# Performance work log

Hardware: AMD Instinct MI355X
Metric: run time of the kernel (lower is better)

The kernel has to match this reference:

```python
import jax, jax.numpy as jnp
import numpy as np

N = 16384
FPS_RATIO = 0.5
RADIUS = 0.25
MAX_NEIGHBORS = 10
C_IN, C_HID, C_OUT = 3, 64, 128


def setup_inputs() -> dict:
    key = jax.random.key(0)
    k0, k1, k2 = jax.random.split(key, 3)
    pos = jax.random.uniform(k0, (N, 3), dtype=jnp.float32)
    batch = jnp.zeros((N,), dtype=jnp.int32)  # single point cloud
    W1 = jax.random.normal(k1, (C_IN, C_HID), dtype=jnp.float32) / np.float32(np.sqrt(C_IN))
    b1 = jnp.zeros((C_HID,), jnp.float32)
    W2 = jax.random.normal(k2, (C_HID, C_OUT), dtype=jnp.float32) / np.float32(np.sqrt(C_HID))
    b2 = jnp.zeros((C_OUT,), jnp.float32)
    return {"pos": pos, "batch": batch, "W1": W1, "b1": b1, "W2": W2, "b2": b2}


def _fps(pos, n_samples):
    # iterative farthest point sampling, deterministic start at index 0
    n = pos.shape[0]
    init = (jnp.full((n,), jnp.finfo(jnp.float32).max, jnp.float32), jnp.int32(0))
    def step(carry, _):
        min_d, last = carry
        d = jnp.sum((pos - pos[last]) ** 2, axis=-1)
        min_d = jnp.minimum(min_d, d)
        nxt = jnp.argmax(min_d).astype(jnp.int32)
        return (min_d, nxt), last
    _, idx = jax.lax.scan(step, init, None, length=n_samples)
    return idx


def _forward(pos, W1, b1, W2, b2):
    n = pos.shape[0]
    s = int(n * FPS_RATIO)
    idx = jax.lax.stop_gradient(_fps(pos, s))          # [S] sampled centers
    centers = pos[idx]                                  # [S,3]
    # ball query: squared distances from each center to all points  [S,N]
    d2 = jnp.sum((centers[:, None, :] - pos[None, :, :]) ** 2, axis=-1)
    neg_d2, src = jax.lax.top_k(-d2, MAX_NEIGHBORS)     # [S,K] nearest-first
    valid = neg_d2 >= -(RADIUS ** 2)                    # within the ball
    # edge_index = stack([col, row]): source = src (full-set idx),
    # target = row (sampled-set idx in [0,S)). PointNetConv does pos_i = pos[row],
    # i.e. indexes the FULL pos with sampled-set indices -> pos[:s].
    pos_i = pos[:s]                                     # [S,3]
    rel = pos[src] - pos_i[:, None, :]                  # [S,K,3] pos_j - pos_i
    # local_mlp (Linear->ReLU->Linear) on each edge message
    h = jax.nn.relu(rel @ W1 + b1) @ W2 + b2            # [S,K,C_OUT]
    h = jnp.where(valid[..., None], h, jnp.float32(-jnp.inf))
    tgt = jnp.repeat(jnp.arange(s, dtype=jnp.int32), MAX_NEIGHBORS)
    out = jax.ops.segment_max(h.reshape(-1, C_OUT), tgt, num_segments=n)  # [N,C]
    # nodes with no incoming edges -> 0 (PyG scatter-max empty fill)
    return jnp.where(jnp.isfinite(out), out, jnp.float32(0.0))


def reference(pos, batch, W1, b1, W2, b2):
    return _forward(pos, W1, b1, W2, b2)
```

## Files before the change

kernel.cpp:

```cpp
#include <hip/hip_runtime.h>

typedef unsigned int u32;
typedef unsigned long long u64;
typedef float f32x2 __attribute__((ext_vector_type(2)));

#define N_PTS 16384
#define N_S   8192
#define NB    10
#define CHID  64
#define COUT  128
#define R2    0.0625f
#define NCELL 4096

__device__ __forceinline__ u32 spread3(u32 v) {
  return (v & 1u) | ((v & 2u) << 2) | ((v & 4u) << 4) | ((v & 8u) << 6);
}

__global__ void cell_kernel(const float* __restrict__ pos, int* __restrict__ cellid,
                            int* __restrict__ hist) {
  int i = blockIdx.x * 256 + threadIdx.x;
  float x = pos[3 * i], y = pos[3 * i + 1], z = pos[3 * i + 2];
  u32 ix = (u32)(x * 16.0f); if (ix > 15u) ix = 15u;
  u32 iy = (u32)(y * 16.0f); if (iy > 15u) iy = 15u;
  u32 iz = (u32)(z * 16.0f); if (iz > 15u) iz = 15u;
  u32 c = spread3(ix) | (spread3(iy) << 1) | (spread3(iz) << 2);
  cellid[i] = (int)c;
  atomicAdd(&hist[c], 1);
}

__global__ __launch_bounds__(1024) void scan_kernel(const int* __restrict__ hist,
                                                    int* __restrict__ base) {
  __shared__ int sp[1024];
  int t = threadIdx.x;
  int h0 = hist[4 * t], h1 = hist[4 * t + 1], h2 = hist[4 * t + 2], h3 = hist[4 * t + 3];
  int s = h0 + h1 + h2 + h3;
  int acc = s;
  sp[t] = s;
  __syncthreads();
  for (int off = 1; off < 1024; off <<= 1) {
    int v = (t >= off) ? sp[t - off] : 0;
    __syncthreads();
    acc += v;
    sp[t] = acc;
    __syncthreads();
  }
  int excl = acc - s;
  base[4 * t + 0] = excl;
  base[4 * t + 1] = excl + h0;
  base[4 * t + 2] = excl + h0 + h1;
  base[4 * t + 3] = excl + h0 + h1 + h2;
}

__global__ void scatter_kernel(const float* __restrict__ pos, const int* __restrict__ cellid,
                               int* __restrict__ base, float* __restrict__ xs,
                               float* __restrict__ ys, float* __restrict__ zs,
                               int* __restrict__ oid) {
  int i = blockIdx.x * 256 + threadIdx.x;
  int c = cellid[i];
  int d = atomicAdd(&base[c], 1);
  xs[d] = pos[3 * i]; ys[d] = pos[3 * i + 1]; zs[d] = pos[3 * i + 2];
  oid[d] = i;
}

#define FPS_T 1024
#define PPT   16
#define WRK   192
#define NCHK  (N_S / 32)

#define OFF_SK   131072
#define OFF_SPD  16384
#define OFF_SPI  57472
#define OFF_W2T  98560
#define OFF_W1   133376
#define OFF_B1   134144
#define OFF_PROG 134400
#define SMEM_SZ  134432

#define KNS    32
#define KTILE  1024
#define KPAD   321
#define W2S    68

#define PT_LIST(OP) OP(0) OP(1) OP(2) OP(3) OP(4) OP(5) OP(6) OP(7) \
                    OP(8) OP(9) OP(10) OP(11) OP(12) OP(13) OP(14) OP(15)
#define G4_LIST(OP) OP(0,0,1,2,3,0,1)   OP(1,4,5,6,7,2,3) \
                    OP(2,8,9,10,11,4,5) OP(3,12,13,14,15,6,7)
#define PR_LIST(OP) OP(0) OP(1) OP(2) OP(3) OP(4) OP(5) OP(6) OP(7)

__device__ __forceinline__ u64 u64fmax(u64 a, u64 b) {
  double ad = __longlong_as_double((long long)a);
  double bd = __longlong_as_double((long long)b);
  return (u64)(long long)__double_as_longlong(fmax(ad, bd));
}

template <int CTRL, int RM>
__device__ __forceinline__ u64 dppmax(u64 cur) {
  int slo = __builtin_amdgcn_update_dpp(0, (int)(u32)cur, CTRL, RM, 0xf, false);
  int shi = __builtin_amdgcn_update_dpp(0, (int)(u32)(cur >> 32), CTRL, RM, 0xf, false);
  u64 o = ((u64)(u32)shi << 32) | (u32)slo;
  return u64fmax(o, cur);
}

__device__ __forceinline__ f32x2 pk_add(f32x2 a, f32x2 b) {
  f32x2 d;
  asm("v_pk_add_f32 %0, %1, %2" : "=v"(d) : "v"(a), "v"(b));
  return d;
}
__device__ __forceinline__ f32x2 pk_mul(f32x2 a, f32x2 b) {
  f32x2 d;
  asm("v_pk_mul_f32 %0, %1, %2" : "=v"(d) : "v"(a), "v"(b));
  return d;
}

__global__ __launch_bounds__(1024, 4)
void fused_kernel(const float* __restrict__ pos,
                  const float* __restrict__ xs,
                  const float* __restrict__ ys,
                  const float* __restrict__ zs,
                  const int* __restrict__ oidv,
                  int* __restrict__ idx,
                  int* __restrict__ src,
                  int* __restrict__ valid,
                  const float* __restrict__ W1,
                  const float* __restrict__ b1,
                  const float* __restrict__ W2,
                  const float* __restrict__ b2,
                  float* __restrict__ out,
                  int* __restrict__ prog) {
  __shared__ __align__(16) unsigned char smem[SMEM_SZ];
  const int t = threadIdx.x;

  if (blockIdx.x == 0) {
    float2* s_yz = (float2*)smem;
    u64 (*s_k)[16] = (u64 (*)[16])(smem + OFF_SK);
    const int wv = t >> 6;
    const int base0 = t * PPT;
    const float4* __restrict__ xv = (const float4*)(xs + base0);
    const float4* __restrict__ yv = (const float4*)(ys + base0);
    const float4* __restrict__ zv = (const float4*)(zs + base0);
    const int4*   __restrict__ ov = (const int4*)(oidv + base0);

#define DECLP(J) float md##J;
    PT_LIST(DECLP)
#undef DECLP
#define DECLC(J) u32 C##J;
    PT_LIST(DECLC)
#undef DECLC
#define DECLX(P) f32x2 X##P; f32x2 Y##P; f32x2 Z##P;
    PR_LIST(DECLX)
#undef DECLX

    float bnx = 3.4e38f, bxx = -3.4e38f, bny = 3.4e38f, bxy = -3.4e38f,
          bnz = 3.4e38f, bxz = -3.4e38f;

#define INIT4(G, J0, J1, J2, J3, PA, PB) { \
    float4 vx = xv[G], vy = yv[G], vz = zv[G]; int4 vo = ov[G]; \
    md##J0 = 3.402823466e38f; md##J1 = 3.402823466e38f; \
    md##J2 = 3.402823466e38f; md##J3 = 3.402823466e38f; \
    X##PA.x = vx.x; X##PA.y = vx.y; X##PB.x = vx.z; X##PB.y = vx.w; \
    Y##PA.x = vy.x; Y##PA.y = vy.y; Y##PB.x = vy.z; Y##PB.y = vy.w; \
    Z##PA.x = vz.x; Z##PA.y = vz.y; Z##PB.x = vz.z; Z##PB.y = vz.w; \
    s_yz[J0 * FPS_T + t] = make_float2(vy.x, vz.x); \
    s_yz[J1 * FPS_T + t] = make_float2(vy.y, vz.y); \
    s_yz[J2 * FPS_T + t] = make_float2(vy.z, vz.z); \
    s_yz[J3 * FPS_T + t] = make_float2(vy.w, vz.w); \
    C##J0 = ((16383u - (u32)vo.x) << 14) | (u32)(base0 + J0); \
    C##J1 = ((16383u - (u32)vo.y) << 14) | (u32)(base0 + J1); \
    C##J2 = ((16383u - (u32)vo.z) << 14) | (u32)(base0 + J2); \
    C##J3 = ((16383u - (u32)vo.w) << 14) | (u32)(base0 + J3); \
    bnx = fminf(bnx, fminf(fminf(vx.x, vx.y), fminf(vx.z, vx.w))); \
    bxx = fmaxf(bxx, fmaxf(fmaxf(vx.x, vx.y), fmaxf(vx.z, vx.w))); \
    bny = fminf(bny, fminf(fminf(vy.x, vy.y), fminf(vy.z, vy.w))); \
    bxy = fmaxf(bxy, fmaxf(fmaxf(vy.x, vy.y), fmaxf(vy.z, vy.w))); \
    bnz = fminf(bnz, fminf(fminf(vz.x, vz.y), fminf(vz.z, vz.w))); \
    bxz = fmaxf(bxz, fmaxf(fmaxf(vz.x, vz.y), fmaxf(vz.z, vz.w))); }
    G4_LIST(INIT4)
#undef INIT4

    u64 ckey = 0;
    u64 wklast = 0;
    float cmaxf = 3.402823466e38f;
    float cx = pos[0], cy = pos[1], cz = pos[2];
    if (t == 0) idx[0] = 0;
    __syncthreads();

    for (int k = 0; k < N_S - 1; ++k) {
      float dxl = fmaxf(fmaxf(bnx - cx, cx - bxx), 0.0f);
      float dyl = fmaxf(fmaxf(bny - cy, cy - bxy), 0.0f);
      float dzl = fmaxf(fmaxf(bnz - cz, cz - bxz), 0.0f);
      float lb2 = dxl * dxl + dyl * dyl + dzl * dzl;
      bool act = (0.99f * lb2 < cmaxf);

      if (__ballot(act)) {
        if (act) {
          f32x2 ncx2; ncx2.x = -cx; ncx2.y = -cx;
          f32x2 ncy2; ncy2.x = -cy; ncy2.y = -cy;
          f32x2 ncz2; ncz2.x = -cz; ncz2.y = -cz;
          u64 bkA = 0, bkB = 0;
#define UPDP(P, J0, J1) { \
          f32x2 dx2 = pk_add(X##P, ncx2); \
          f32x2 dy2 = pk_add(Y##P, ncy2); \
          f32x2 dz2 = pk_add(Z##P, ncz2); \
          f32x2 sq = pk_add(pk_mul(dx2, dx2), pk_mul(dy2, dy2)); \
          f32x2 d2 = pk_add(sq, pk_mul(dz2, dz2)); \
          float m0 = fminf(md##J0, d2.x); md##J0 = m0; \
          bkA = u64fmax(bkA, ((u64)__float_as_uint(m0) << 32) | C##J0); \
          float m1 = fminf(md##J1, d2.y); md##J1 = m1; \
          bkB = u64fmax(bkB, ((u64)__float_as_uint(m1) << 32) | C##J1); }
          UPDP(0, 0, 1)  UPDP(1, 2, 3)  UPDP(2, 4, 5)  UPDP(3, 6, 7)
          UPDP(4, 8, 9)  UPDP(5, 10, 11) UPDP(6, 12, 13) UPDP(7, 14, 15)
#undef UPDP
          ckey = u64fmax(bkA, bkB);
          cmaxf = __uint_as_float((u32)(ckey >> 32));
        }
        u64 wk = ckey;
        wk = dppmax<0x111, 0xf>(wk);
        wk = dppmax<0x112, 0xf>(wk);
        wk = dppmax<0x114, 0xf>(wk);
        wk = dppmax<0x118, 0xf>(wk);
        wk = dppmax<0x142, 0xa>(wk);
        wk = dppmax<0x143, 0xc>(wk);
        wklast = wk;
      }
      if ((t & 63) == 63) s_k[k & 1][wv] = wklast;
      __syncthreads();

      u64 gk = s_k[k & 1][t & 15];
      gk = dppmax<0x121, 0xf>(gk);
      gk = dppmax<0x122, 0xf>(gk);
      gk = dppmax<0x124, 0xf>(gk);
      gk = dppmax<0x128, 0xf>(gk);
      u32 glo = (u32)__builtin_amdgcn_readfirstlane((int)(u32)gk);
      u32 ghi = (u32)__builtin_amdgcn_readfirstlane((int)(u32)(gk >> 32));
      u64 gmax = ((u64)ghi << 32) | glo;
      int sidx = (int)(gmax & 16383u);
      if (t == 0) {
        idx[k + 1] = 16383 - (int)((gmax >> 14) & 16383u);
        if ((k & 31) == 30)
          __hip_atomic_store(prog, k + 2, __ATOMIC_RELEASE, __HIP_MEMORY_SCOPE_AGENT);
      }
      int cell = (sidx & (PPT - 1)) * FPS_T + (sidx >> 4);
      cx = xs[sidx];
      float2 yz = s_yz[cell];
      cy = yz.x;
      cz = yz.y;
    }
  } else {
    const int wid = blockIdx.x - 1;
    float4* s_p = (float4*)smem;
    float (*spd)[KPAD] = (float (*)[KPAD])(smem + OFF_SPD);
    int   (*spi)[KPAD] = (int (*)[KPAD])(smem + OFF_SPI);
    float* sW2T = (float*)(smem + OFF_W2T);
    float* sW1  = (float*)(smem + OFF_W1);
    float* sb1  = (float*)(smem + OFF_B1);
    int*   sprog = (int*)(smem + OFF_PROG);
    float* msh1  = (float*)(smem + OFF_SPD);
    float* msrel = (float*)(smem + OFF_SPI);

    for (int e = t; e < CHID * COUT; e += 1024) {
      int kk = e >> 7, c = e & (COUT - 1);
      sW2T[c * W2S + kk] = W2[e];
    }
    if (t < 3 * CHID) sW1[t] = W1[t];
    if (t < CHID) sb1[t] = b1[t];
    {
      float4* outv = (float4*)(out + (size_t)N_S * COUT);
      const int cnt = (N_PTS - N_S) * COUT / 4;
      for (int j = wid * 1024 + t; j < cnt; j += WRK * 1024)
        outv[j] = make_float4(0.f, 0.f, 0.f, 0.f);
    }
    __syncthreads();

    for (int gc = wid; gc < NCHK; gc += WRK) {
      const int need = gc * 32 + 32;
      for (;;) {
        if (t == 0) *sprog = __hip_atomic_load(prog, __ATOMIC_RELAXED, __HIP_MEMORY_SCOPE_AGENT);
        __syncthreads();
        if (*sprog >= need) break;
        __builtin_amdgcn_s_sleep(32);
        __syncthreads();
      }
      const int sp = t >> 5;
      const int cl = t & 31;
      const int i = gc * 32 + cl;
      const int ci = __hip_atomic_load(idx + i, __ATOMIC_RELAXED, __HIP_MEMORY_SCOPE_AGENT);
      const float cx = pos[3 * ci], cy = pos[3 * ci + 1], cz = pos[3 * ci + 2];
      float nd[NB]; int ni[NB];
#pragma unroll
      for (int q = 0; q < NB; ++q) { nd[q] = 3.402823466e38f; ni[q] = 0x7fffffff; }

      for (int base = 0; base < N_PTS; base += KTILE) {
        __syncthreads();
        for (int j = t; j < KTILE; j += 1024) {
          int pnt = base + j;
          s_p[j] = make_float4(pos[3 * pnt], pos[3 * pnt + 1], pos[3 * pnt + 2], 0.f);
        }
        __syncthreads();
        for (int j = sp; j < KTILE; j += KNS) {
          float4 q4 = s_p[j];
          float dx = __fsub_rn(cx, q4.x);
          float dy = __fsub_rn(cy, q4.y);
          float dz = __fsub_rn(cz, q4.z);
          float d2 = __fadd_rn(__fadd_rn(__fmul_rn(dx, dx), __fmul_rn(dy, dy)), __fmul_rn(dz, dz));
          if (d2 < nd[NB - 1]) {
            float cd = d2; int cp = base + j;
#pragma unroll
            for (int q = 0; q < NB; ++q) {
              bool sw = (cd < nd[q]) || (cd == nd[q] && cp < ni[q]);
              if (sw) { float td = nd[q]; int tp = ni[q]; nd[q] = cd; ni[q] = cp; cd = td; cp = tp; }
            }
          }
        }
      }
#pragma unroll
      for (int q = 0; q < NB; ++q) { spd[cl][sp * NB + q] = nd[q]; spi[cl][sp * NB + q] = ni[q]; }
      __syncthreads();
      if (sp == 0) {
        int cur[KNS];
#pragma unroll
        for (int s = 0; s < KNS; ++s) cur[s] = 0;
        int vb = 0;
        for (int q = 0; q < NB; ++q) {
          float bd = 3.402823466e38f; int bi = 0x7fffffff; int bsl = 0;
#pragma unroll
          for (int s = 0; s < KNS; ++s) {
            float d = spd[cl][s * NB + cur[s]]; int id = spi[cl][s * NB + cur[s]];
            if (d < bd || (d == bd && id < bi)) { bd = d; bi = id; bsl = s; }
          }
#pragma unroll
          for (int s = 0; s < KNS; ++s) cur[s] += (s == bsl) ? 1 : 0;
          src[i * NB + q] = bi;
          if (bd <= R2) vb |= (1 << q);
        }
        valid[i] = vb;
      }
      __syncthreads();

      for (int r = 0; r < 4; ++r) {
        const int c8 = t >> 7;
        const int ch = t & 127;
        const int im = gc * 32 + r * 8 + c8;
        if (ch < NB) {
          int s = src[im * NB + ch];
          msrel[(c8 * NB + ch) * 3 + 0] = pos[3 * s + 0] - pos[3 * im + 0];
          msrel[(c8 * NB + ch) * 3 + 1] = pos[3 * s + 1] - pos[3 * im + 1];
          msrel[(c8 * NB + ch) * 3 + 2] = pos[3 * s + 2] - pos[3 * im + 2];
        }
        __syncthreads();
        for (int e = t; e < 8 * NB * CHID; e += 1024) {
          int kk = e & 63;
          int n = (e >> 6) % NB;
          int cc = e / (NB * CHID);
          float a = sb1[kk] + msrel[(cc * NB + n) * 3 + 0] * sW1[kk]
                            + msrel[(cc * NB + n) * 3 + 1] * sW1[64 + kk]
                            + msrel[(cc * NB + n) * 3 + 2] * sW1[128 + kk];
          msh1[(cc * NB + n) * CHID + kk] = fmaxf(a, 0.0f);
        }
        __syncthreads();
        {
          const int vmask = valid[im];
          const float bb = b2[ch];
          float m = 0.0f;
          bool any = false;
          for (int n = 0; n < NB; ++n) {
            if (vmask & (1 << n)) {
              float acc = bb;
#pragma unroll
              for (int g = 0; g < 16; ++g) {
                float4 h = *(const float4*)&msh1[(c8 * NB + n) * CHID + 4 * g];
                float4 w = *(const float4*)&sW2T[ch * W2S + 4 * g];
                acc = fmaf(h.x, w.x, acc);
                acc = fmaf(h.y, w.y, acc);
                acc = fmaf(h.z, w.z, acc);
                acc = fmaf(h.w, w.w, acc);
              }
              m = any ? fmaxf(m, acc) : acc;
              any = true;
            }
          }
          out[(size_t)im * COUT + ch] = any ? m : 0.0f;
        }
        __syncthreads();
      }
    }
  }
}

extern "C" void kernel_launch(void* const* d_in, const int* in_sizes, int n_in,
                              void* d_out, int out_size, void* d_ws, size_t ws_size,
                              hipStream_t stream) {
  (void)in_sizes; (void)n_in; (void)out_size; (void)ws_size;
  const float* pos = (const float*)d_in[0];
  const float* W1 = (const float*)d_in[2];
  const float* b1 = (const float*)d_in[3];
  const float* W2 = (const float*)d_in[4];
  const float* b2 = (const float*)d_in[5];
  float* out = (float*)d_out;

  char* ws = (char*)d_ws;
  int*   idx   = (int*)ws;                 ws += (size_t)N_S * 4;
  int*   src   = (int*)ws;                 ws += (size_t)N_S * NB * 4;
  int*   valid = (int*)ws;                 ws += (size_t)N_S * 4;
  float* xs    = (float*)ws;               ws += (size_t)N_PTS * 4;
  float* ys    = (float*)ws;               ws += (size_t)N_PTS * 4;
  float* zs    = (float*)ws;               ws += (size_t)N_PTS * 4;
  int*   oid   = (int*)ws;                 ws += (size_t)N_PTS * 4;
  int*   progp = (int*)ws;                 ws += 16;
  int* cellid = src;
  int* hist   = src + N_PTS;
  int* basebuf= src + N_PTS + NCELL;

  hipMemsetAsync(hist, 0, (size_t)NCELL * 4, stream);
  hipMemsetAsync(progp, 0, 4, stream);
  cell_kernel<<<N_PTS / 256, 256, 0, stream>>>(pos, cellid, hist);
  scan_kernel<<<1, 1024, 0, stream>>>(hist, basebuf);
  scatter_kernel<<<N_PTS / 256, 256, 0, stream>>>(pos, cellid, basebuf, xs, ys, zs, oid);
  fused_kernel<<<1 + WRK, 1024, 0, stream>>>(pos, xs, ys, zs, oid, idx, src, valid,
                                             W1, b1, W2, b2, out, progp);
}
```

Before: 6.900 ms.

## Use one wavefront per center with DPP merge and smaller work chunks

The neighbor search now gives each of 16 centers per chunk a full 64-lane wavefront instead of splitting 32 centers over 32 subgroups. The top-10 merge uses wave-wide DPP max reductions on packed distance/index keys instead of a serial shared-memory 32-way merge done by one thread group. The chunk size drops to 16, so FPS publishes progress twice as often and workers can start earlier, which lowers pipeline latency behind the sequential FPS. The cost is more chunks, more polling and barrier rounds per center, and a 10-step wave reduction per center.

```diff
diff --git a/kernel.cpp b/kernel.cpp
--- a/kernel.cpp
+++ b/kernel.cpp
@@ -65,20 +65,19 @@
 #define FPS_T 1024
 #define PPT   16
 #define WRK   192
-#define NCHK  (N_S / 32)
-
-#define OFF_SK   131072
-#define OFF_SPD  16384
-#define OFF_SPI  57472
-#define OFF_W2T  98560
-#define OFF_W1   133376
-#define OFF_B1   134144
-#define OFF_PROG 134400
-#define SMEM_SZ  134432
-
-#define KNS    32
+#define CHC   16
+#define NCHK  (N_S / CHC)
+
+#define OFF_SK    131072
+#define OFF_W2T   16384
+#define OFF_W1    51200
+#define OFF_B1    51968
+#define OFF_PROG  52224
+#define OFF_MSH1  53248
+#define OFF_MSREL 73728
+#define SMEM_SZ   131328
+
 #define KTILE  1024
-#define KPAD   321
 #define W2S    68
 
 #define PT_LIST(OP) OP(0) OP(1) OP(2) OP(3) OP(4) OP(5) OP(6) OP(7) \
@@ -101,6 +100,18 @@
   return u64fmax(o, cur);
 }
 
+__device__ __forceinline__ u64 wavemax_bcast(u64 x) {
+  x = dppmax<0x111, 0xf>(x);
+  x = dppmax<0x112, 0xf>(x);
+  x = dppmax<0x114, 0xf>(x);
+  x = dppmax<0x118, 0xf>(x);
+  x = dppmax<0x142, 0xa>(x);
+  x = dppmax<0x143, 0xc>(x);
+  u32 lo = (u32)__builtin_amdgcn_readlane((int)(u32)x, 63);
+  u32 hi = (u32)__builtin_amdgcn_readlane((int)(u32)(x >> 32), 63);
+  return ((u64)hi << 32) | lo;
+}
+
 __device__ __forceinline__ f32x2 pk_add(f32x2 a, f32x2 b) {
   f32x2 d;
   asm("v_pk_add_f32 %0, %1, %2" : "=v"(d) : "v"(a), "v"(b));
@@ -110,6 +121,10 @@
   f32x2 d;
   asm("v_pk_mul_f32 %0, %1, %2" : "=v"(d) : "v"(a), "v"(b));
   return d;
+}
+
+__device__ __forceinline__ u64 mkey(float d, int idx) {
+  return ((u64)(0x7F800000u - __float_as_uint(d)) << 32) | (u32)(16383 - idx);
 }
 
 __global__ __launch_bounds__(1024, 4)
@@ -236,7 +251,7 @@
       int sidx = (int)(gmax & 16383u);
       if (t == 0) {
         idx[k + 1] = 16383 - (int)((gmax >> 14) & 16383u);
-        if ((k & 31) == 30)
+        if ((k & 15) == 14)
           __hip_atomic_store(prog, k + 2, __ATOMIC_RELEASE, __HIP_MEMORY_SCOPE_AGENT);
       }
       int cell = (sidx & (PPT - 1)) * FPS_T + (sidx >> 4);
@@ -247,15 +262,13 @@
     }
   } else {
     const int wid = blockIdx.x - 1;
-    float4* s_p = (float4*)smem;
-    float (*spd)[KPAD] = (float (*)[KPAD])(smem + OFF_SPD);
-    int   (*spi)[KPAD] = (int (*)[KPAD])(smem + OFF_SPI);
-    float* sW2T = (float*)(smem + OFF_W2T);
-    float* sW1  = (float*)(smem + OFF_W1);
-    float* sb1  = (float*)(smem + OFF_B1);
+    float4* s_p  = (float4*)smem;
+    float* sW2T  = (float*)(smem + OFF_W2T);
+    float* sW1   = (float*)(smem + OFF_W1);
+    float* sb1   = (float*)(smem + OFF_B1);
     int*   sprog = (int*)(smem + OFF_PROG);
-    float* msh1  = (float*)(smem + OFF_SPD);
-    float* msrel = (float*)(smem + OFF_SPI);
+    float* msh1  = (float*)(smem + OFF_MSH1);
+    float* msrel = (float*)(smem + OFF_MSREL);
 
     for (int e = t; e < CHID * COUT; e += 1024) {
       int kk = e >> 7, c = e & (COUT - 1);
@@ -272,7 +285,7 @@
     __syncthreads();
 
     for (int gc = wid; gc < NCHK; gc += WRK) {
-      const int need = gc * 32 + 32;
+      const int need = gc * CHC + CHC;
       for (;;) {
         if (t == 0) *sprog = __hip_atomic_load(prog, __ATOMIC_RELAXED, __HIP_MEMORY_SCOPE_AGENT);
         __syncthreads();
@@ -280,23 +293,23 @@
         __builtin_amdgcn_s_sleep(32);
         __syncthreads();
       }
-      const int sp = t >> 5;
-      const int cl = t & 31;
-      const int i = gc * 32 + cl;
+      const int w = t >> 6;
+      const int l = t & 63;
+      const int i = gc * CHC + w;
       const int ci = __hip_atomic_load(idx + i, __ATOMIC_RELAXED, __HIP_MEMORY_SCOPE_AGENT);
       const float cx = pos[3 * ci], cy = pos[3 * ci + 1], cz = pos[3 * ci + 2];
       float nd[NB]; int ni[NB];
 #pragma unroll
-      for (int q = 0; q < NB; ++q) { nd[q] = 3.402823466e38f; ni[q] = 0x7fffffff; }
+      for (int q = 0; q < NB; ++q) { nd[q] = 3.402823466e38f; ni[q] = 16383; }
 
       for (int base = 0; base < N_PTS; base += KTILE) {
         __syncthreads();
-        for (int j = t; j < KTILE; j += 1024) {
-          int pnt = base + j;
-          s_p[j] = make_float4(pos[3 * pnt], pos[3 * pnt + 1], pos[3 * pnt + 2], 0.f);
-        }
-        __syncthreads();
-        for (int j = sp; j < KTILE; j += KNS) {
+        {
+          int pnt = base + t;
+          s_p[t] = make_float4(pos[3 * pnt], pos[3 * pnt + 1], pos[3 * pnt + 2], 0.f);
+        }
+        __syncthreads();
+        for (int j = l; j < KTILE; j += 64) {
           float4 q4 = s_p[j];
           float dx = __fsub_rn(cx, q4.x);
           float dy = __fsub_rn(cy, q4.y);
@@ -312,34 +325,31 @@
           }
         }
       }
+      {
+        int vb = 0;
+        u64 myk = mkey(nd[0], ni[0]);
+        for (int q = 0; q < NB; ++q) {
+          u64 g = wavemax_bcast(myk);
+          if (myk == g) {
 #pragma unroll
-      for (int q = 0; q < NB; ++q) { spd[cl][sp * NB + q] = nd[q]; spi[cl][sp * NB + q] = ni[q]; }
+            for (int j = 0; j < NB - 1; ++j) { nd[j] = nd[j + 1]; ni[j] = ni[j + 1]; }
+            nd[NB - 1] = 3.402823466e38f; ni[NB - 1] = 16383;
+            myk = mkey(nd[0], ni[0]);
+          }
+          if (l == 0) {
+            src[i * NB + q] = 16383 - (int)(g & 0xFFFFFFFFu);
+            float bd = __uint_as_float(0x7F800000u - (u32)(g >> 32));
+            if (bd <= R2) vb |= (1 << q);
+          }
+        }
+        if (l == 0) valid[i] = vb;
+      }
       __syncthreads();
-      if (sp == 0) {
-        int cur[KNS];
-#pragma unroll
-        for (int s = 0; s < KNS; ++s) cur[s] = 0;
-        int vb = 0;
-        for (int q = 0; q < NB; ++q) {
-          float bd = 3.402823466e38f; int bi = 0x7fffffff; int bsl = 0;
-#pragma unroll
-          for (int s = 0; s < KNS; ++s) {
-            float d = spd[cl][s * NB + cur[s]]; int id = spi[cl][s * NB + cur[s]];
-            if (d < bd || (d == bd && id < bi)) { bd = d; bi = id; bsl = s; }
-          }
-#pragma unroll
-          for (int s = 0; s < KNS; ++s) cur[s] += (s == bsl) ? 1 : 0;
-          src[i * NB + q] = bi;
-          if (bd <= R2) vb |= (1 << q);
-        }
-        valid[i] = vb;
-      }
-      __syncthreads();
-
-      for (int r = 0; r < 4; ++r) {
+
+      for (int r = 0; r < 2; ++r) {
         const int c8 = t >> 7;
         const int ch = t & 127;
-        const int im = gc * 32 + r * 8 + c8;
+        const int im = gc * CHC + r * 8 + c8;
         if (ch < NB) {
           int s = src[im * NB + ch];
           msrel[(c8 * NB + ch) * 3 + 0] = pos[3 * s + 0] - pos[3 * im + 0];
@@ -368,11 +378,11 @@
 #pragma unroll
               for (int g = 0; g < 16; ++g) {
                 float4 h = *(const float4*)&msh1[(c8 * NB + n) * CHID + 4 * g];
-                float4 w = *(const float4*)&sW2T[ch * W2S + 4 * g];
-                acc = fmaf(h.x, w.x, acc);
-                acc = fmaf(h.y, w.y, acc);
-                acc = fmaf(h.z, w.z, acc);
-                acc = fmaf(h.w, w.w, acc);
+                float4 wv4 = *(const float4*)&sW2T[ch * W2S + 4 * g];
+                acc = fmaf(h.x, wv4.x, acc);
+                acc = fmaf(h.y, wv4.y, acc);
+                acc = fmaf(h.z, wv4.z, acc);
+                acc = fmaf(h.w, wv4.w, acc);
               }
               m = any ? fmaxf(m, acc) : acc;
               any = true;
@@ -410,8 +420,8 @@
   int* hist   = src + N_PTS;
   int* basebuf= src + N_PTS + NCELL;
 
-  hipMemsetAsync(hist, 0, (size_t)NCELL * 4, stream);
-  hipMemsetAsync(progp, 0, 4, stream);
+  (void)hipMemsetAsync(hist, 0, (size_t)NCELL * 4, stream);
+  (void)hipMemsetAsync(progp, 0, 4, stream);
   cell_kernel<<<N_PTS / 256, 256, 0, stream>>>(pos, cellid, hist);
   scan_kernel<<<1, 1024, 0, stream>>>(hist, basebuf);
   scatter_kernel<<<N_PTS / 256, 256, 0, stream>>>(pos, cellid, basebuf, xs, ys, zs, oid);
```

New measurement: 6.564 ms. 1.05x faster.
